# Kernel optimization log

Hardware: AMD Instinct MI355X
Metric: run time of the kernel (lower is better)

The kernel has to match this reference:

```python
import jax, jax.numpy as jnp
import numpy as np

B, S, D = 2, 2048, 1024
H = 16
HD = D // H  # 64
SCALE = HD ** 0.5


def setup_inputs() -> dict:
    key = jax.random.key(0)
    ks = jax.random.split(key, 9)
    std = 1.0 / np.sqrt(D)
    inp = {"x": jax.random.normal(ks[0], (B, S, D), dtype=jnp.float32)}
    names = ["Wq", "Wk", "Wv", "Wo"]
    for i, n in enumerate(names):
        inp[n] = jax.random.uniform(ks[1 + i], (D, D), dtype=jnp.float32, minval=-std, maxval=std)
        inp["b" + n[1]] = jax.random.uniform(ks[5 + i], (D,), dtype=jnp.float32, minval=-std, maxval=std)
    return inp


def reference(x, Wq, Wk, Wv, Wo, bq, bk, bv, bo):
    # QKV projections (torch Linear: y = x @ W.T + b; here W stored as [in, out] already transposed)
    q = x @ Wq + bq
    k = x @ Wk + bk
    v = x @ Wv + bv
    # [B, H, S, HD]
    q = q.reshape(B, S, H, HD).transpose(0, 2, 1, 3)
    k = k.reshape(B, S, H, HD).transpose(0, 2, 1, 3)
    v = v.reshape(B, S, H, HD).transpose(0, 2, 1, 3)
    scores = jnp.einsum("bhqd,bhkd->bhqk", q, k) / SCALE  # [B, H, S, S]
    causal = jnp.tril(jnp.ones((S, S), dtype=bool))
    scores = jnp.where(causal, scores, -jnp.inf)
    attn = jax.nn.softmax(scores, axis=-1)  # dropout p=0.0 (eval)
    ctx = jnp.einsum("bhqk,bhkd->bhqd", attn, v)
    ctx = ctx.transpose(0, 2, 1, 3).reshape(B, S, D)
    return ctx @ Wo + bo
```

## Files before the change

### kernel.cpp

```cpp
#include <hip/hip_runtime.h>


#define S_LEN 2048
#define DMODEL 1024
#define NHEAD 16
#define HDIM 64
#define MROWS 4096

typedef __bf16 bf16x8 __attribute__((ext_vector_type(8)));
typedef float f32x4 __attribute__((ext_vector_type(4)));
typedef float f32x16 __attribute__((ext_vector_type(16)));

__device__ __forceinline__ ushort f2bf(float f) {
  union { float f; unsigned u; } v; v.f = f;
  unsigned r = v.u + 0x7fffu + ((v.u >> 16) & 1u);
  return (ushort)(r >> 16);
}

__device__ __forceinline__ void gload_lds16(const ushort* g, ushort* l) {
  __builtin_amdgcn_global_load_lds(
      (const __attribute__((address_space(1))) void*)g,
      (__attribute__((address_space(3))) void*)l, 16, 0, 0);
}

__device__ __forceinline__ unsigned pack2bf(float lo, float hi) {
  union { __bf16 h[2]; unsigned u; } t;
  t.h[0] = (__bf16)lo; t.h[1] = (__bf16)hi;
  return t.u;
}

#if __has_builtin(__builtin_amdgcn_permlane32_swap)
#define HAVE_PL32 1
__device__ __forceinline__ void pl32sw(unsigned& a, unsigned& b) {
  auto r = __builtin_amdgcn_permlane32_swap((int)a, (int)b, false, false);
  a = (unsigned)r[0];
  b = (unsigned)r[1];
}
#endif

__device__ __forceinline__ float halfcomb_max(float x) {
#ifdef HAVE_PL32
  unsigned a = __float_as_uint(x), b = a;
  pl32sw(a, b);
  return fmaxf(__uint_as_float(a), __uint_as_float(b));
#else
  return fmaxf(x, __shfl_xor(x, 32, 64));
#endif
}
__device__ __forceinline__ float halfcomb_sum(float x) {
#ifdef HAVE_PL32
  unsigned a = __float_as_uint(x), b = a;
  pl32sw(a, b);
  return __uint_as_float(a) + __uint_as_float(b);
#else
  return x + __shfl_xor(x, 32, 64);
#endif
}


__global__ __launch_bounds__(256) void cvt_x(const float* __restrict__ x,
                                             ushort* __restrict__ xb) {
  int i = (blockIdx.x * 256 + threadIdx.x) * 4;
  float4 v = *(const float4*)&x[i];
  ushort4 o;
  o.x = f2bf(v.x); o.y = f2bf(v.y); o.z = f2bf(v.z); o.w = f2bf(v.w);
  *(ushort4*)&xb[i] = o;
}

__global__ __launch_bounds__(256) void cvt_wt(const float* __restrict__ W0,
                                              const float* __restrict__ W1,
                                              const float* __restrict__ W2,
                                              const float* __restrict__ W3,
                                              ushort* __restrict__ out) {
  const float* W = blockIdx.z == 0 ? W0 : blockIdx.z == 1 ? W1
                   : blockIdx.z == 2 ? W2 : W3;
  ushort* WT = out + (size_t)blockIdx.z * DMODEL * DMODEL;
  __shared__ float tile[32][33];
  int n0 = blockIdx.x * 32, k0 = blockIdx.y * 32;
  int tx = threadIdx.x & 31, ty = threadIdx.x >> 5;
#pragma unroll
  for (int i = 0; i < 32; i += 8)
    tile[ty + i][tx] = W[(size_t)(k0 + ty + i) * DMODEL + n0 + tx];
  __syncthreads();
#pragma unroll
  for (int i = 0; i < 32; i += 8)
    WT[(size_t)(n0 + ty + i) * DMODEL + k0 + tx] = f2bf(tile[tx][ty + i]);
}

__global__ __launch_bounds__(256) void trV(const ushort* __restrict__ V,
                                           ushort* __restrict__ Vt) {
  const int bh = blockIdx.z;
  const ushort* src = V + (size_t)bh * S_LEN * HDIM;
  ushort* dst = Vt + (size_t)bh * HDIM * S_LEN;
  __shared__ ushort tile[32][33];
  int s0 = blockIdx.x * 32, h0 = blockIdx.y * 32;
  int tx = threadIdx.x & 31, ty = threadIdx.x >> 5;
#pragma unroll
  for (int i = 0; i < 32; i += 8)
    tile[ty + i][tx] = src[(size_t)(s0 + ty + i) * HDIM + h0 + tx];
  __syncthreads();
#pragma unroll
  for (int i = 0; i < 32; i += 8)
    dst[(size_t)(h0 + ty + i) * S_LEN + s0 + tx] = tile[tx][ty + i];
}

__global__ __launch_bounds__(512) void gemm256(
    const ushort* __restrict__ A, const ushort* __restrict__ Bt,
    const float* __restrict__ b0, const float* __restrict__ b1,
    const float* __restrict__ b2, ushort* __restrict__ outQ,
    ushort* __restrict__ outK, ushort* __restrict__ outV) {
  const int flat = blockIdx.y * 16 + blockIdx.x;
  const int swz = (flat & 7) * 24 + (flat >> 3);
  const int bx = swz & 15, by = swz >> 4;
  const int m0 = bx * 256, n0 = by * 256;

  __shared__ __align__(16) ushort Al[2][256 * 64];
  __shared__ __align__(16) ushort Bl[2][256 * 64];

  const int tid = threadIdx.x;
  const int lane = tid & 63, wid = tid >> 6;
  const int wr = wid >> 2, wc = wid & 3;
  const int fr = lane & 15, hi16 = lane >> 4;

  f32x4 acc[8][4] = {};

#pragma unroll
  for (int l = 0; l < 4; ++l) {
    int chunk = l * 512 + tid;
    int row = chunk >> 3, cpos = chunk & 7;
    int scol = (cpos ^ (row & 7)) * 8;
    gload_lds16(&A[(size_t)(m0 + row) * DMODEL + scol], &Al[0][chunk * 8]);
    gload_lds16(&Bt[(size_t)(n0 + row) * DMODEL + scol], &Bl[0][chunk * 8]);
  }
  __syncthreads();

  for (int t = 0; t < 16; ++t) {
    const int bt = t & 1;
    bf16x8 bfr[4];
#pragma unroll
    for (int s = 0; s < 4; ++s) {
      const int kk = s >> 1, mh = s & 1;
      bf16x8 af[4];
#pragma unroll
      for (int q = 0; q < 4; ++q) {
        int rl = wr * 128 + (mh * 4 + q) * 16 + fr;
        af[q] = *(const bf16x8*)&Al[bt][rl * 64 +
                                        ((kk * 4 + hi16) ^ (rl & 7)) * 8];
      }
      if (mh == 0) {
#pragma unroll
        for (int nf = 0; nf < 4; ++nf) {
          int rl = wc * 64 + nf * 16 + fr;
          bfr[nf] = *(const bf16x8*)&Bl[bt][rl * 64 +
                                            ((kk * 4 + hi16) ^ (rl & 7)) * 8];
        }
      }
      if (t + 1 < 16 && s < 2) {
        const int k64 = (t + 1) * 64;
#pragma unroll
        for (int l = 0; l < 4; ++l) {
          int chunk = l * 512 + tid;
          int row = chunk >> 3, cpos = chunk & 7;
          int scol = (cpos ^ (row & 7)) * 8;
          if (s == 0)
            gload_lds16(&A[(size_t)(m0 + row) * DMODEL + k64 + scol],
                        &Al[bt ^ 1][chunk * 8]);
          else
            gload_lds16(&Bt[(size_t)(n0 + row) * DMODEL + k64 + scol],
                        &Bl[bt ^ 1][chunk * 8]);
        }
      }
      __builtin_amdgcn_s_barrier();
      __builtin_amdgcn_s_setprio(1);
#pragma unroll
      for (int q = 0; q < 4; ++q)
#pragma unroll
        for (int nf = 0; nf < 4; ++nf)
          acc[mh * 4 + q][nf] = __builtin_amdgcn_mfma_f32_16x16x32_bf16(
              af[q], bfr[nf], acc[mh * 4 + q][nf], 0, 0, 0);
      __builtin_amdgcn_s_setprio(0);
      if (s < 3) __builtin_amdgcn_s_barrier();
    }
    __syncthreads();
  }

#pragma unroll
  for (int mf = 0; mf < 8; ++mf) {
#pragma unroll
    for (int nf = 0; nf < 4; ++nf) {
      int col = n0 + wc * 64 + nf * 16 + fr;
      int z = col >> 10, cw = col & 1023;
      float bval = z == 0 ? b0[cw] : z == 1 ? b1[cw] : b2[cw];
      int h = cw >> 6, hd = cw & (HDIM - 1);
      ushort* dst = (z == 0) ? outQ : (z == 1) ? outK : outV;
#pragma unroll
      for (int rg = 0; rg < 4; ++rg) {
        int row = m0 + wr * 128 + mf * 16 + hi16 * 4 + rg;
        int b = row >> 11, sq = row & (S_LEN - 1);
        float val = acc[mf][nf][rg] + bval;
        dst[(((size_t)(b * NHEAD + h)) * S_LEN + sq) * HDIM + hd] = f2bf(val);
      }
    }
  }
}

__global__ __launch_bounds__(256) void gemm128o(
    const ushort* __restrict__ A, const ushort* __restrict__ Bt,
    const float* __restrict__ b0, float* __restrict__ outB) {
  const int NT = 256;
  const int flat = blockIdx.y * 32 + blockIdx.x;
  const int swz = (flat & 7) * (NT >> 3) + (flat >> 3);
  const int bx = swz & 31, by = swz >> 5;
  const int m0 = bx * 128, n0 = by * 128;

  __shared__ __align__(16) ushort Alds[2][128 * 64];
  __shared__ __align__(16) ushort Blds[2][128 * 64];

  const int tid = threadIdx.x;
  const int lane = tid & 63, w = tid >> 6;
  const int wr = w >> 1, wc = w & 1;
  const int fr = lane & 15, hi16 = lane >> 4;

  f32x4 acc[4][4] = {};

  auto STAGE = [&](int kt, int bi) {
#pragma unroll
    for (int it = 0; it < 4; ++it) {
      int c = it * 256 + tid;
      int row = c >> 3;
      int sc = ((c & 7) ^ (row & 7)) * 8;
      int ldsbase = (it * 256 + w * 64) * 8;
      gload_lds16(&A[(size_t)(m0 + row) * DMODEL + kt + sc],
                  &Alds[bi][ldsbase]);
      gload_lds16(&Bt[(size_t)(n0 + row) * DMODEL + kt + sc],
                  &Blds[bi][ldsbase]);
    }
  };

  auto COMPUTE = [&](int bi) {
#pragma unroll
    for (int kk = 0; kk < 2; ++kk) {
      bf16x8 af[4], bfr[4];
#pragma unroll
      for (int i = 0; i < 4; ++i) {
        int row = wr * 64 + i * 16 + fr;
        af[i] = *(const bf16x8*)&Alds[bi][row * 64 +
                                          ((kk * 4 + hi16) ^ (row & 7)) * 8];
      }
#pragma unroll
      for (int j = 0; j < 4; ++j) {
        int row = wc * 64 + j * 16 + fr;
        bfr[j] = *(const bf16x8*)&Blds[bi][row * 64 +
                                           ((kk * 4 + hi16) ^ (row & 7)) * 8];
      }
#pragma unroll
      for (int i = 0; i < 4; ++i)
#pragma unroll
        for (int j = 0; j < 4; ++j)
          acc[i][j] = __builtin_amdgcn_mfma_f32_16x16x32_bf16(af[i], bfr[j],
                                                              acc[i][j], 0, 0, 0);
    }
  };

  STAGE(0, 0);
  __syncthreads();
  int buf = 0;
  for (int kt = 64; kt < DMODEL; kt += 64) {
    STAGE(kt, buf ^ 1);
    COMPUTE(buf);
    __syncthreads();
    buf ^= 1;
  }
  COMPUTE(buf);

#pragma unroll
  for (int i = 0; i < 4; ++i) {
#pragma unroll
    for (int j = 0; j < 4; ++j) {
      int col = n0 + wc * 64 + j * 16 + fr;
      float bval = b0[col];
#pragma unroll
      for (int r = 0; r < 4; ++r) {
        int row = m0 + wr * 64 + i * 16 + hi16 * 4 + r;
        outB[(size_t)row * DMODEL + col] = acc[i][j][r] + bval;
      }
    }
  }
}

__global__ __launch_bounds__(256, 2) void attn4(const ushort* __restrict__ Q,
                                                const ushort* __restrict__ K,
                                                const ushort* __restrict__ Vt,
                                                ushort* __restrict__ ctx) {
  const int n = blockIdx.x;
  const int v = (n & 7) * 64 + (n >> 3);
  const int ptile = v & 15, bh = v >> 4;
  const int b = bh >> 4, h = bh & 15;
  const int tid = threadIdx.x;
  const int lane = tid & 63, wid = tid >> 6;
  const int p = wid >> 1;
  const int wq = wid & 1;
  const int q32 = lane & 31, hi = lane >> 5;
  const bool lo_half = (hi == 0);
  const int tid2 = tid & 127;

  const ushort* Qb = Q + (size_t)bh * S_LEN * HDIM;
  const ushort* Kb = K + (size_t)bh * S_LEN * HDIM;
  const ushort* Vb = Vt + (size_t)bh * HDIM * S_LEN;

  __shared__ __align__(16) ushort Kl[2][2][64 * 64];
  __shared__ __align__(16) ushort Vl[2][2][64 * 64];
  float* scr = (float*)&Kl[0][0][0];

  const float C = 0.125f * 1.44269504f;

  for (int ph = 0; ph < 2; ++ph) {
    const int j = ph ? 31 - ptile : ptile;
    const int qbase = j * 64 + wq * 32;
    const int qrow = qbase + q32;

    bf16x8 qf[4];
#pragma unroll
    for (int s = 0; s < 4; ++s)
      qf[s] = *(const bf16x8*)&Qb[(size_t)qrow * HDIM + s * 16 + hi * 8];

    f32x16 oacc[2] = {};
    float mraw = -1e30f, lsum = 0.f;
    const int NS = (j >> 1) + 1;

    if (p <= j) {
      const int kv = p * 64;
#pragma unroll
      for (int it = 0; it < 4; ++it) {
        int chunk = it * 128 + tid2;
        int row = chunk >> 3, sc = ((chunk & 7) ^ (row & 7)) * 8;
        gload_lds16(&Kb[(size_t)(kv + row) * HDIM + sc], &Kl[p][0][chunk * 8]);
        gload_lds16(&Vb[(size_t)row * S_LEN + kv + sc], &Vl[p][0][chunk * 8]);
      }
    }
    __syncthreads();

    int buf = 0;
    for (int it = 0; it < NS; ++it) {
      const int s = 2 * it + p;
      const int kv0 = s * 64;

      if (s + 2 <= j) {
        const int kvn = kv0 + 128;
#pragma unroll
        for (int st = 0; st < 4; ++st) {
          int chunk = st * 128 + tid2;
          int row = chunk >> 3, sc = ((chunk & 7) ^ (row & 7)) * 8;
          gload_lds16(&Kb[(size_t)(kvn + row) * HDIM + sc],
                      &Kl[p][buf ^ 1][chunk * 8]);
          gload_lds16(&Vb[(size_t)row * S_LEN + kvn + sc],
                      &Vl[p][buf ^ 1][chunk * 8]);
        }
      }

      if (s <= j) {
        f32x16 sa[2] = {};
        __builtin_amdgcn_s_setprio(1);
#pragma unroll
        for (int t = 0; t < 2; ++t) {
          const int row = t * 32 + q32;
          const int rsw = (row & 7);
#pragma unroll
          for (int sl = 0; sl < 4; ++sl) {
            bf16x8 kf = *(const bf16x8*)&Kl[p][buf][row * 64 +
                                                    ((sl * 2 + hi) ^ rsw) * 8];
            sa[t] = __builtin_amdgcn_mfma_f32_32x32x16_bf16(kf, qf[sl], sa[t],
                                                            0, 0, 0);
          }
        }
        __builtin_amdgcn_s_setprio(0);

        bf16x8 vf[2][4];
#pragma unroll
        for (int t2 = 0; t2 < 2; ++t2) {
          const int row = t2 * 32 + q32;
          const int rsw = (row & 7);
#pragma unroll
          for (int sl = 0; sl < 4; ++sl)
            vf[t2][sl] = *(const bf16x8*)&Vl[p][buf][row * 64 +
                                                     ((sl * 2 + hi) ^ rsw) * 8];
        }

        if (kv0 + 63 > qbase) {
          const int khi = kv0 + 4 * hi;
#pragma unroll
          for (int t = 0; t < 2; ++t)
#pragma unroll
            for (int r = 0; r < 16; ++r) {
              int kg = khi + t * 32 + (r & 3) + 8 * (r >> 2);
              if (kg > qrow) sa[t][r] = -1e30f;
            }
        }

        float tmv[8];
#pragma unroll
        for (int r = 0; r < 8; ++r)
          tmv[r] = fmaxf(fmaxf(sa[0][r], sa[0][r + 8]),
                         fmaxf(sa[1][r], sa[1][r + 8]));
        float t0 = fmaxf(fmaxf(tmv[0], tmv[1]), fmaxf(tmv[2], tmv[3]));
        float t1 = fmaxf(fmaxf(tmv[4], tmv[5]), fmaxf(tmv[6], tmv[7]));
        float tm = halfcomb_max(fmaxf(t0, t1));

        if (!__all(tm <= mraw + 64.f)) {
          float mnew = fmaxf(mraw, tm);
          float alpha = __builtin_exp2f((mraw - mnew) * C);
          lsum *= alpha;
#pragma unroll
          for (int r = 0; r < 16; ++r) { oacc[0][r] *= alpha; oacc[1][r] *= alpha; }
          mraw = mnew;
        }
        const float mC = mraw * C;
        float psum = 0.f;
#pragma unroll
        for (int t = 0; t < 2; ++t)
#pragma unroll
          for (int r = 0; r < 16; ++r) {
            float pp = __builtin_exp2f(__builtin_fmaf(sa[t][r], C, -mC));
            sa[t][r] = pp;
            psum += pp;
          }
        lsum += halfcomb_sum(psum);

        __builtin_amdgcn_s_setprio(1);
#pragma unroll
        for (int t = 0; t < 2; ++t) {
#pragma unroll
          for (int half = 0; half < 2; ++half) {
            const int rb = half * 8;
            unsigned a0 = pack2bf(sa[t][rb + 0], sa[t][rb + 1]);
            unsigned a1 = pack2bf(sa[t][rb + 2], sa[t][rb + 3]);
            unsigned b0w = pack2bf(sa[t][rb + 4], sa[t][rb + 5]);
            unsigned b1w = pack2bf(sa[t][rb + 6], sa[t][rb + 7]);
            union { unsigned u[4]; bf16x8 v; } pf;
#ifdef HAVE_PL32
            pl32sw(a0, b0w);
            pl32sw(a1, b1w);
            pf.u[0] = a0; pf.u[1] = a1; pf.u[2] = b0w; pf.u[3] = b1w;
#else
            unsigned xa0 = __shfl_xor(a0, 32, 64);
            unsigned xa1 = __shfl_xor(a1, 32, 64);
            unsigned xb0 = __shfl_xor(b0w, 32, 64);
            unsigned xb1 = __shfl_xor(b1w, 32, 64);
            pf.u[0] = lo_half ? a0 : xb0;
            pf.u[1] = lo_half ? a1 : xb1;
            pf.u[2] = lo_half ? xa0 : b0w;
            pf.u[3] = lo_half ? xa1 : b1w;
#endif
            oacc[0] = __builtin_amdgcn_mfma_f32_32x32x16_bf16(
                vf[0][t * 2 + half], pf.v, oacc[0], 0, 0, 0);
            oacc[1] = __builtin_amdgcn_mfma_f32_32x32x16_bf16(
                vf[1][t * 2 + half], pf.v, oacc[1], 0, 0, 0);
          }
        }
        __builtin_amdgcn_s_setprio(0);
      }

      __syncthreads();
      buf ^= 1;
    }

    const int base = (wq * 64 + lane) * 37;
    if (p == 1) {
      scr[base + 0] = mraw;
      scr[base + 1] = lsum;
#pragma unroll
      for (int t = 0; t < 2; ++t)
#pragma unroll
        for (int r = 0; r < 16; ++r) scr[base + 2 + t * 16 + r] = oacc[t][r];
    }
    __syncthreads();
    if (p == 0) {
      const float mB = scr[base + 0], lB = scr[base + 1];
      const float mS = fmaxf(mraw, mB);
      const float aA = __builtin_exp2f((mraw - mS) * C);
      const float aB = __builtin_exp2f((mB - mS) * C);
      const float lT = lsum * aA + lB * aB;
      const float linv = 1.0f / lT;
      ushort* crow = &ctx[((size_t)(b * S_LEN) + qrow) * DMODEL + h * HDIM];
#pragma unroll
      for (int t = 0; t < 2; ++t)
#pragma unroll
        for (int g2 = 0; g2 < 4; ++g2) {
          ushort4 o;
          float m0 = oacc[t][g2 * 4 + 0] * aA + scr[base + 2 + t * 16 + g2 * 4 + 0] * aB;
          float m1 = oacc[t][g2 * 4 + 1] * aA + scr[base + 2 + t * 16 + g2 * 4 + 1] * aB;
          float m2 = oacc[t][g2 * 4 + 2] * aA + scr[base + 2 + t * 16 + g2 * 4 + 2] * aB;
          float m3 = oacc[t][g2 * 4 + 3] * aA + scr[base + 2 + t * 16 + g2 * 4 + 3] * aB;
          o.x = f2bf(m0 * linv); o.y = f2bf(m1 * linv);
          o.z = f2bf(m2 * linv); o.w = f2bf(m3 * linv);
          *(ushort4*)&crow[t * 32 + g2 * 8 + hi * 4] = o;
        }
    }
    __syncthreads();
  }
}


extern "C" void kernel_launch(void* const* d_in, const int* in_sizes, int n_in,
                              void* d_out, int out_size, void* d_ws,
                              size_t ws_size, hipStream_t stream) {
  const float* x  = (const float*)d_in[0];
  const float* Wq = (const float*)d_in[1];
  const float* bq = (const float*)d_in[2];
  const float* Wk = (const float*)d_in[3];
  const float* bk = (const float*)d_in[4];
  const float* Wv = (const float*)d_in[5];
  const float* bv = (const float*)d_in[6];
  const float* Wo = (const float*)d_in[7];
  const float* bo = (const float*)d_in[8];

  char* ws = (char*)d_ws;
  ushort* Xbf = (ushort*)ws;
  ushort* WT  = (ushort*)(ws + (size_t)8 * 1024 * 1024);
  ushort* QKV = (ushort*)(ws + (size_t)16 * 1024 * 1024);
  ushort* CTX = (ushort*)(ws + (size_t)40 * 1024 * 1024);

  const size_t QKV_ELEMS = (size_t)MROWS * DMODEL;
  const size_t W_ELEMS = (size_t)DMODEL * DMODEL;

  ushort* Qp  = QKV;
  ushort* Kp  = QKV + QKV_ELEMS;
  ushort* Vtp = QKV + 2 * QKV_ELEMS;
  ushort* Vrp = CTX;

  cvt_x<<<4096, 256, 0, stream>>>(x, Xbf);
  cvt_wt<<<dim3(32, 32, 4), 256, 0, stream>>>(Wq, Wk, Wv, Wo, WT);
  gemm256<<<dim3(16, 12), 512, 0, stream>>>(Xbf, WT, bq, bk, bv, Qp, Kp, Vrp);
  trV<<<dim3(64, 2, 32), 256, 0, stream>>>(Vrp, Vtp);
  attn4<<<dim3(512), 256, 0, stream>>>(Qp, Kp, Vtp, CTX);
  gemm128o<<<dim3(32, 8), 256, 0, stream>>>(CTX, WT + 3 * W_ELEMS, bo,
                                            (float*)d_out);
}
```

Before: 126.7 us.

## Retile QKV GEMM to 256x192 for 256 blocks and vectorize weight transpose

The fused QKV GEMM tile shrinks from 256x256 to 256x192 columns, so the grid grows from 192 to 256 workgroups to fill the GPU's compute units more evenly. The swizzle, B-tile loads, fragment counts and epilogue are adjusted to match. Separately, the weight transpose-and-convert kernel now uses 64x64 tiles with float4 loads and ushort4 stores. The cost is lower per-block arithmetic intensity and more B-operand reloads per output element.

```diff
diff --git a/kernel.cpp b/kernel.cpp
--- a/kernel.cpp
+++ b/kernel.cpp
@@ -75,16 +75,26 @@
   const float* W = blockIdx.z == 0 ? W0 : blockIdx.z == 1 ? W1
                    : blockIdx.z == 2 ? W2 : W3;
   ushort* WT = out + (size_t)blockIdx.z * DMODEL * DMODEL;
-  __shared__ float tile[32][33];
-  int n0 = blockIdx.x * 32, k0 = blockIdx.y * 32;
-  int tx = threadIdx.x & 31, ty = threadIdx.x >> 5;
-#pragma unroll
-  for (int i = 0; i < 32; i += 8)
-    tile[ty + i][tx] = W[(size_t)(k0 + ty + i) * DMODEL + n0 + tx];
+  __shared__ float tile[64][65];
+  const int n0 = blockIdx.x * 64, k0 = blockIdx.y * 64;
+#pragma unroll
+  for (int i = 0; i < 4; ++i) {
+    int chunk = i * 256 + threadIdx.x;
+    int r = chunk >> 4, c4 = chunk & 15;
+    float4 v = *(const float4*)&W[(size_t)(k0 + r) * DMODEL + n0 + c4 * 4];
+    tile[r][c4 * 4 + 0] = v.x; tile[r][c4 * 4 + 1] = v.y;
+    tile[r][c4 * 4 + 2] = v.z; tile[r][c4 * 4 + 3] = v.w;
+  }
   __syncthreads();
 #pragma unroll
-  for (int i = 0; i < 32; i += 8)
-    WT[(size_t)(n0 + ty + i) * DMODEL + k0 + tx] = f2bf(tile[tx][ty + i]);
+  for (int i = 0; i < 4; ++i) {
+    int chunk = i * 256 + threadIdx.x;
+    int r = chunk >> 4, c4 = chunk & 15;
+    ushort4 o;
+    o.x = f2bf(tile[c4 * 4 + 0][r]); o.y = f2bf(tile[c4 * 4 + 1][r]);
+    o.z = f2bf(tile[c4 * 4 + 2][r]); o.w = f2bf(tile[c4 * 4 + 3][r]);
+    *(ushort4*)&WT[(size_t)(n0 + r) * DMODEL + k0 + c4 * 4] = o;
+  }
 }
 
 __global__ __launch_bounds__(256) void trV(const ushort* __restrict__ V,
@@ -110,19 +120,19 @@
     const float* __restrict__ b2, ushort* __restrict__ outQ,
     ushort* __restrict__ outK, ushort* __restrict__ outV) {
   const int flat = blockIdx.y * 16 + blockIdx.x;
-  const int swz = (flat & 7) * 24 + (flat >> 3);
+  const int swz = (flat & 7) * 32 + (flat >> 3);
   const int bx = swz & 15, by = swz >> 4;
-  const int m0 = bx * 256, n0 = by * 256;
+  const int m0 = bx * 256, n0 = by * 192;
 
   __shared__ __align__(16) ushort Al[2][256 * 64];
-  __shared__ __align__(16) ushort Bl[2][256 * 64];
+  __shared__ __align__(16) ushort Bl[2][192 * 64];
 
   const int tid = threadIdx.x;
   const int lane = tid & 63, wid = tid >> 6;
   const int wr = wid >> 2, wc = wid & 3;
   const int fr = lane & 15, hi16 = lane >> 4;
 
-  f32x4 acc[8][4] = {};
+  f32x4 acc[8][3] = {};
 
 #pragma unroll
   for (int l = 0; l < 4; ++l) {
@@ -130,13 +140,19 @@
     int row = chunk >> 3, cpos = chunk & 7;
     int scol = (cpos ^ (row & 7)) * 8;
     gload_lds16(&A[(size_t)(m0 + row) * DMODEL + scol], &Al[0][chunk * 8]);
+  }
+#pragma unroll
+  for (int l = 0; l < 3; ++l) {
+    int chunk = l * 512 + tid;
+    int row = chunk >> 3, cpos = chunk & 7;
+    int scol = (cpos ^ (row & 7)) * 8;
     gload_lds16(&Bt[(size_t)(n0 + row) * DMODEL + scol], &Bl[0][chunk * 8]);
   }
   __syncthreads();
 
   for (int t = 0; t < 16; ++t) {
     const int bt = t & 1;
-    bf16x8 bfr[4];
+    bf16x8 bfr[3];
 #pragma unroll
     for (int s = 0; s < 4; ++s) {
       const int kk = s >> 1, mh = s & 1;
@@ -149,25 +165,32 @@
       }
       if (mh == 0) {
 #pragma unroll
-        for (int nf = 0; nf < 4; ++nf) {
-          int rl = wc * 64 + nf * 16 + fr;
+        for (int nf = 0; nf < 3; ++nf) {
+          int rl = wc * 48 + nf * 16 + fr;
           bfr[nf] = *(const bf16x8*)&Bl[bt][rl * 64 +
                                             ((kk * 4 + hi16) ^ (rl & 7)) * 8];
         }
       }
       if (t + 1 < 16 && s < 2) {
         const int k64 = (t + 1) * 64;
-#pragma unroll
-        for (int l = 0; l < 4; ++l) {
-          int chunk = l * 512 + tid;
-          int row = chunk >> 3, cpos = chunk & 7;
-          int scol = (cpos ^ (row & 7)) * 8;
-          if (s == 0)
+        if (s == 0) {
+#pragma unroll
+          for (int l = 0; l < 4; ++l) {
+            int chunk = l * 512 + tid;
+            int row = chunk >> 3, cpos = chunk & 7;
+            int scol = (cpos ^ (row & 7)) * 8;
             gload_lds16(&A[(size_t)(m0 + row) * DMODEL + k64 + scol],
                         &Al[bt ^ 1][chunk * 8]);
-          else
+          }
+        } else {
+#pragma unroll
+          for (int l = 0; l < 3; ++l) {
+            int chunk = l * 512 + tid;
+            int row = chunk >> 3, cpos = chunk & 7;
+            int scol = (cpos ^ (row & 7)) * 8;
             gload_lds16(&Bt[(size_t)(n0 + row) * DMODEL + k64 + scol],
                         &Bl[bt ^ 1][chunk * 8]);
+          }
         }
       }
       __builtin_amdgcn_s_barrier();
@@ -175,7 +198,7 @@
 #pragma unroll
       for (int q = 0; q < 4; ++q)
 #pragma unroll
-        for (int nf = 0; nf < 4; ++nf)
+        for (int nf = 0; nf < 3; ++nf)
           acc[mh * 4 + q][nf] = __builtin_amdgcn_mfma_f32_16x16x32_bf16(
               af[q], bfr[nf], acc[mh * 4 + q][nf], 0, 0, 0);
       __builtin_amdgcn_s_setprio(0);
@@ -187,8 +210,8 @@
 #pragma unroll
   for (int mf = 0; mf < 8; ++mf) {
 #pragma unroll
-    for (int nf = 0; nf < 4; ++nf) {
-      int col = n0 + wc * 64 + nf * 16 + fr;
+    for (int nf = 0; nf < 3; ++nf) {
+      int col = n0 + wc * 48 + nf * 16 + fr;
       int z = col >> 10, cw = col & 1023;
       float bval = z == 0 ? b0[cw] : z == 1 ? b1[cw] : b2[cw];
       int h = cw >> 6, hd = cw & (HDIM - 1);
@@ -529,8 +552,8 @@
   ushort* Vrp = CTX;
 
   cvt_x<<<4096, 256, 0, stream>>>(x, Xbf);
-  cvt_wt<<<dim3(32, 32, 4), 256, 0, stream>>>(Wq, Wk, Wv, Wo, WT);
-  gemm256<<<dim3(16, 12), 512, 0, stream>>>(Xbf, WT, bq, bk, bv, Qp, Kp, Vrp);
+  cvt_wt<<<dim3(16, 16, 4), 256, 0, stream>>>(Wq, Wk, Wv, Wo, WT);
+  gemm256<<<dim3(16, 16), 512, 0, stream>>>(Xbf, WT, bq, bk, bv, Qp, Kp, Vrp);
   trV<<<dim3(64, 2, 32), 256, 0, stream>>>(Vrp, Vtp);
   attn4<<<dim3(512), 256, 0, stream>>>(Qp, Kp, Vtp, CTX);
   gemm128o<<<dim3(32, 8), 256, 0, stream>>>(CTX, WT + 3 * W_ELEMS, bo,
```

New measurement: 122.0 us. -3.7%, faster.
